# Kernel optimization log

Hardware: AMD Instinct MI355X
Metric: run time of the kernel (lower is better)

## Reference

```python
import jax, jax.numpy as jnp
import numpy as np

# Lens/CCD constants from the source module
DX = 0.00859375
F = 8.0
OX = 5.5 / 2.0   # CCD_width / 2
OY = 7.7 / 2.0   # CCD_length / 2

B, C, H, W = 4, 3, 1024, 2048


def _make_bn(h, w):
    # bn[i, j] = floor((cos(atan(dx*(j-ox)/f)) - 1) * (i - oy)), as in __init__
    j = np.arange(w, dtype=np.float64)
    i = np.arange(h, dtype=np.float64)
    a0 = np.arctan(DX * (j - OX) / F)
    bn = np.floor((np.cos(a0)[None, :] - 1.0) * (i[:, None] - OY))
    return bn.astype(np.int32)


def setup_inputs() -> dict:
    key = jax.random.key(0)
    k1, k2 = jax.random.split(key)
    x = jax.random.normal(k1, (B, C, H, W), dtype=jnp.float32)
    # Conv2d(3, 3, kernel_size=3, bias=False) weight: (out_c, in_c, kh, kw)
    weight = jax.random.normal(k2, (3, 3, 3, 3), dtype=jnp.float32) * 0.1
    bn = jnp.asarray(_make_bn(H, W))  # int32 distortion LUT, shape (H, W)
    return {"x": x, "weight": weight, "bn": bn}


def reference(x, weight, bn):
    B_, C_, H_, W_ = x.shape
    Hi, Wj = H_ - 2, W_ // 2 - 2  # active region: i+2 < H and j+2 < W//2
    i = jnp.arange(Hi)
    j = jnp.arange(Wj)
    p = jnp.arange(3)  # k // 3 (patch row)
    q = jnp.arange(3)  # k % 3  (patch col)
    # column used for the LUT wraps for j >= 256 (j1 = j % 256)
    j1 = jnp.where(j >= 256, j % 256, j)
    rows = i[:, None] + p[None, :]        # (Hi, 3)
    cols = j1[:, None] + q[None, :]       # (Wj, 3)
    # tb(i, j, p, q) = i + p + bn[i + p, j1 + q]
    bn_sel = bn[rows[:, None, :, None], cols[None, :, None, :]]  # (Hi, Wj, 3, 3)
    R = rows[:, None, :, None] + bn_sel                          # source row indices
    # Faithful quirk from the source: patch column index into input is q (0..2),
    # NOT j + q: matrix1[:, :, p, q] = input[:, :, tb, q]
    gathered = x[:, :, R, q]  # (B, C, Hi, Wj, 3, 3)
    out_act = jnp.einsum('bcijpq,ocpq->boij', gathered, weight)  # per-pixel 3x3 conv
    # guard from the source: only write when i + 2 + bn[i+2, j+2] < H
    mask = (i[:, None] + 2 + bn[i[:, None] + 2, j[None, :] + 2]) < H_
    out_act = out_act * mask.astype(out_act.dtype)
    return jnp.zeros((B_, C_, H_, W_), x.dtype).at[:, :, :Hi, :Wj].set(out_act)
```

## Files before the change

### kernel.cpp

```cpp
#include <hip/hip_runtime.h>


#define HH 1024
#define WW 2048
#define HI 1022
#define WJ 1022
#define XSPAN 64

typedef float f32x4 __attribute__((ext_vector_type(4)));
typedef int   i32x4 __attribute__((ext_vector_type(4)));

__global__ __launch_bounds__(256) void dis_conv_kernel(
    const float* __restrict__ x,
    const float* __restrict__ w,
    const int*   __restrict__ bn,
    float*       __restrict__ out)
{
    const int bi = blockIdx.x;
    const int b  = bi >> 10;
    const int i  = bi & 1023;
    const int t  = threadIdx.x;

    __shared__ __align__(16) float v[3][256];
    __shared__ __align__(16) float xs[3][XSPAN][4];
    __shared__ __align__(16) int   bn01[2][260];
    __shared__ __align__(16) int   bn2[1032];

    const int   j4 = t * 4;
    const f32x4 z  = (f32x4)(0.f);

    #pragma unroll
    for (int o = 0; o < 3; ++o) {
        float* orow = out + (((size_t)(b * 3 + o)) * HH + i) * WW;
        __builtin_nontemporal_store(z, (f32x4*)&orow[j4 + 1024]);
    }

    const bool activeRow = (i < HI);
    const int  lo        = (i > 61) ? (i - 61) : 0;

    if (activeRow) {
        ((i32x4*)bn2)[t] = ((const i32x4*)(bn + (size_t)(i + 2) * WW))[t];
        if (t < 130) {
            const int p = (t >= 65) ? 1 : 0;
            const int k = t - p * 65;
            ((i32x4*)&bn01[p][0])[k] =
                ((const i32x4*)(bn + (size_t)(i + p) * WW))[k];
        }
        if (t < 192) {
            const int c = t >> 6;
            const int r = t & 63;
            const f32x4 xv =
                *(const f32x4*)(x + ((size_t)(b * 3 + c) * HH + (lo + r)) * WW);
            xs[0][r][c] = xv[0];
            xs[1][r][c] = xv[1];
            xs[2][r][c] = xv[2];
        }
    }
    __syncthreads();

    float acc0 = 0.f, acc1 = 0.f, acc2 = 0.f;
    if (activeRow) {
        int  rr[3][3];
        bool ok = true;
        #pragma unroll
        for (int p = 0; p < 3; ++p) {
            #pragma unroll
            for (int q = 0; q < 3; ++q) {
                const int bv = (p < 2) ? bn01[p][t + q] : bn2[t + q];
                rr[p][q] = i + p + bv - lo;
                ok &= ((unsigned)rr[p][q] < XSPAN);
            }
        }
        if (__builtin_expect(ok, 1)) {
            #pragma unroll
            for (int p = 0; p < 3; ++p) {
                #pragma unroll
                for (int q = 0; q < 3; ++q) {
                    const f32x4 g = *(const f32x4*)&xs[q][rr[p][q]][0];
                    #pragma unroll
                    for (int c = 0; c < 3; ++c) {
                        acc0 += g[c] * w[(0 * 3 + c) * 9 + p * 3 + q];
                        acc1 += g[c] * w[(1 * 3 + c) * 9 + p * 3 + q];
                        acc2 += g[c] * w[(2 * 3 + c) * 9 + p * 3 + q];
                    }
                }
            }
        } else {
            #pragma unroll
            for (int c = 0; c < 3; ++c) {
                const float* xbase = x + (size_t)(b * 3 + c) * (HH * WW);
                #pragma unroll
                for (int p = 0; p < 3; ++p) {
                    #pragma unroll
                    for (int q = 0; q < 3; ++q) {
                        int rv = rr[p][q] + lo;
                        if (rv < 0)    rv += HH;
                        if (rv >= HH)  rv -= HH;
                        const float xv = xbase[(size_t)rv * WW + q];
                        acc0 += xv * w[(0 * 3 + c) * 9 + p * 3 + q];
                        acc1 += xv * w[(1 * 3 + c) * 9 + p * 3 + q];
                        acc2 += xv * w[(2 * 3 + c) * 9 + p * 3 + q];
                    }
                }
            }
        }
    }
    v[0][t] = acc0;
    v[1][t] = acc1;
    v[2][t] = acc2;
    __syncthreads();

    f32x4 mm = z;
    if (activeRow) {
        const i32x4 g0 = *(const i32x4*)&bn2[j4];
        const i32x4 g1 = *(const i32x4*)&bn2[j4 + 4];
        const int bv[4] = { g0[2], g0[3], g1[0], g1[1] };
        #pragma unroll
        for (int k = 0; k < 4; ++k) {
            const int j = j4 + k;
            mm[k] = (j < WJ && (i + 2) + bv[k] < HH) ? 1.f : 0.f;
        }
    }
    #pragma unroll
    for (int o = 0; o < 3; ++o) {
        float* orow = out + (((size_t)(b * 3 + o)) * HH + i) * WW;
        const f32x4 vv = *(const f32x4*)&v[o][j4 & 255];
        const f32x4 rv = vv * mm;
        __builtin_nontemporal_store(rv, (f32x4*)&orow[j4]);
    }
}

extern "C" void kernel_launch(void* const* d_in, const int* in_sizes, int n_in,
                              void* d_out, int out_size, void* d_ws, size_t ws_size,
                              hipStream_t stream) {
    const float* x   = (const float*)d_in[0];
    const float* w   = (const float*)d_in[1];
    const int*   bn  = (const int*)d_in[2];
    float*       out = (float*)d_out;

    dis_conv_kernel<<<dim3(4096), dim3(256), 0, stream>>>(x, w, bn, out);
}
```

Baseline: 164.4 us.

## Process all four batches per block to share bn loads and index math

Each block now handles one output row for all four batch images instead of a single batch, so the grid shrinks from 4096 to 1024 blocks. The bn LUT rows and the per-pixel gather indices are loaded and computed once and reused across batches, and the x staging is spread over all 256 threads. This cuts redundant bn traffic and index work, but uses more LDS and registers per block and leaves fewer blocks to hide the store-dominated memory latency.

```diff
diff --git a/kernel.cpp b/kernel.cpp
--- a/kernel.cpp
+++ b/kernel.cpp
@@ -16,13 +16,11 @@
     const int*   __restrict__ bn,
     float*       __restrict__ out)
 {
-    const int bi = blockIdx.x;
-    const int b  = bi >> 10;
-    const int i  = bi & 1023;
-    const int t  = threadIdx.x;
+    const int i = blockIdx.x;
+    const int t = threadIdx.x;
 
-    __shared__ __align__(16) float v[3][256];
-    __shared__ __align__(16) float xs[3][XSPAN][4];
+    __shared__ __align__(16) float v[4][3][256];
+    __shared__ __align__(16) float xs[4][3][XSPAN][4];
     __shared__ __align__(16) int   bn01[2][260];
     __shared__ __align__(16) int   bn2[1032];
 
@@ -30,8 +28,8 @@
     const f32x4 z  = (f32x4)(0.f);
 
     #pragma unroll
-    for (int o = 0; o < 3; ++o) {
-        float* orow = out + (((size_t)(b * 3 + o)) * HH + i) * WW;
+    for (int bo = 0; bo < 12; ++bo) {
+        float* orow = out + ((size_t)bo * HH + i) * WW;
         __builtin_nontemporal_store(z, (f32x4*)&orow[j4 + 1024]);
     }
 
@@ -46,19 +44,29 @@
             ((i32x4*)&bn01[p][0])[k] =
                 ((const i32x4*)(bn + (size_t)(i + p) * WW))[k];
         }
-        if (t < 192) {
-            const int c = t >> 6;
-            const int r = t & 63;
+        #pragma unroll
+        for (int k = 0; k < 3; ++k) {
+            const int idx = t + 256 * k;
+            const int bb  = idx / 192;
+            const int rem = idx - bb * 192;
+            const int c   = rem >> 6;
+            const int r   = rem & 63;
             const f32x4 xv =
-                *(const f32x4*)(x + ((size_t)(b * 3 + c) * HH + (lo + r)) * WW);
-            xs[0][r][c] = xv[0];
-            xs[1][r][c] = xv[1];
-            xs[2][r][c] = xv[2];
+                *(const f32x4*)(x + ((size_t)(bb * 3 + c) * HH + (lo + r)) * WW);
+            xs[bb][0][r][c] = xv[0];
+            xs[bb][1][r][c] = xv[1];
+            xs[bb][2][r][c] = xv[2];
         }
     }
     __syncthreads();
 
-    float acc0 = 0.f, acc1 = 0.f, acc2 = 0.f;
+    float acc[4][3];
+    #pragma unroll
+    for (int bb = 0; bb < 4; ++bb)
+        #pragma unroll
+        for (int o = 0; o < 3; ++o)
+            acc[bb][o] = 0.f;
+
     if (activeRow) {
         int  rr[3][3];
         bool ok = true;
@@ -76,38 +84,47 @@
             for (int p = 0; p < 3; ++p) {
                 #pragma unroll
                 for (int q = 0; q < 3; ++q) {
-                    const f32x4 g = *(const f32x4*)&xs[q][rr[p][q]][0];
+                    const int r = rr[p][q];
                     #pragma unroll
-                    for (int c = 0; c < 3; ++c) {
-                        acc0 += g[c] * w[(0 * 3 + c) * 9 + p * 3 + q];
-                        acc1 += g[c] * w[(1 * 3 + c) * 9 + p * 3 + q];
-                        acc2 += g[c] * w[(2 * 3 + c) * 9 + p * 3 + q];
+                    for (int bb = 0; bb < 4; ++bb) {
+                        const f32x4 g = *(const f32x4*)&xs[bb][q][r][0];
+                        #pragma unroll
+                        for (int c = 0; c < 3; ++c) {
+                            acc[bb][0] += g[c] * w[(0 * 3 + c) * 9 + p * 3 + q];
+                            acc[bb][1] += g[c] * w[(1 * 3 + c) * 9 + p * 3 + q];
+                            acc[bb][2] += g[c] * w[(2 * 3 + c) * 9 + p * 3 + q];
+                        }
                     }
                 }
             }
         } else {
             #pragma unroll
-            for (int c = 0; c < 3; ++c) {
-                const float* xbase = x + (size_t)(b * 3 + c) * (HH * WW);
+            for (int bb = 0; bb < 4; ++bb) {
                 #pragma unroll
-                for (int p = 0; p < 3; ++p) {
+                for (int c = 0; c < 3; ++c) {
+                    const float* xbase = x + (size_t)(bb * 3 + c) * (HH * WW);
                     #pragma unroll
-                    for (int q = 0; q < 3; ++q) {
-                        int rv = rr[p][q] + lo;
-                        if (rv < 0)    rv += HH;
-                        if (rv >= HH)  rv -= HH;
-                        const float xv = xbase[(size_t)rv * WW + q];
-                        acc0 += xv * w[(0 * 3 + c) * 9 + p * 3 + q];
-                        acc1 += xv * w[(1 * 3 + c) * 9 + p * 3 + q];
-                        acc2 += xv * w[(2 * 3 + c) * 9 + p * 3 + q];
+                    for (int p = 0; p < 3; ++p) {
+                        #pragma unroll
+                        for (int q = 0; q < 3; ++q) {
+                            int rv = rr[p][q] + lo;
+                            if (rv < 0)    rv += HH;
+                            if (rv >= HH)  rv -= HH;
+                            const float xv = xbase[(size_t)rv * WW + q];
+                            acc[bb][0] += xv * w[(0 * 3 + c) * 9 + p * 3 + q];
+                            acc[bb][1] += xv * w[(1 * 3 + c) * 9 + p * 3 + q];
+                            acc[bb][2] += xv * w[(2 * 3 + c) * 9 + p * 3 + q];
+                        }
                     }
                 }
             }
         }
     }
-    v[0][t] = acc0;
-    v[1][t] = acc1;
-    v[2][t] = acc2;
+    #pragma unroll
+    for (int bb = 0; bb < 4; ++bb)
+        #pragma unroll
+        for (int o = 0; o < 3; ++o)
+            v[bb][o][t] = acc[bb][o];
     __syncthreads();
 
     f32x4 mm = z;
@@ -122,11 +139,14 @@
         }
     }
     #pragma unroll
-    for (int o = 0; o < 3; ++o) {
-        float* orow = out + (((size_t)(b * 3 + o)) * HH + i) * WW;
-        const f32x4 vv = *(const f32x4*)&v[o][j4 & 255];
-        const f32x4 rv = vv * mm;
-        __builtin_nontemporal_store(rv, (f32x4*)&orow[j4]);
+    for (int bb = 0; bb < 4; ++bb) {
+        #pragma unroll
+        for (int o = 0; o < 3; ++o) {
+            float* orow = out + (((size_t)(bb * 3 + o)) * HH + i) * WW;
+            const f32x4 vv = *(const f32x4*)&v[bb][o][j4 & 255];
+            const f32x4 rv = vv * mm;
+            __builtin_nontemporal_store(rv, (f32x4*)&orow[j4]);
+        }
     }
 }
 
@@ -138,5 +158,5 @@
     const int*   bn  = (const int*)d_in[2];
     float*       out = (float*)d_out;
 
-    dis_conv_kernel<<<dim3(4096), dim3(256), 0, stream>>>(x, w, bn, out);
+    dis_conv_kernel<<<dim3(1024), dim3(256), 0, stream>>>(x, w, bn, out);
 }
```

Result: no change. 166.3 us (+1.2%).
